# Kernel optimization log

Measured on AMD Instinct MI355X. Metric: run time of the kernel, lower is better.

## Reference

```python
import jax, jax.numpy as jnp
import numpy as np

N_NODES = 100000
N_EDGES = 400000
N_GRAPHS = 4096
D = 300          # emb_dim
L = 5            # num_layers
NUM_ATOM, NUM_CHIR = 120, 3
NUM_BOND, NUM_DIR = 6, 3
SELF_LOOP_BOND = 4
TEMP = 0.04


def setup_inputs() -> dict:
    key = jax.random.key(0)
    ks = jax.random.split(key, 24)
    inp = {}
    # graph batch 0
    inp["x0"] = jax.random.randint(ks[0], (N_NODES, 2), 0, 3)
    inp["edge_index0"] = jax.random.randint(ks[1], (2, N_EDGES), 0, N_NODES)
    inp["edge_attr0"] = jax.random.randint(ks[2], (N_EDGES, 2), 0, 3)
    inp["batch_ids0"] = jnp.sort(jax.random.randint(ks[3], (N_NODES,), 0, N_GRAPHS))
    inp["dangling0"] = jax.random.randint(ks[4], (N_GRAPHS,), 0, N_NODES)
    # graph batch 1
    inp["x1"] = jax.random.randint(ks[5], (N_NODES, 2), 0, 3)
    inp["edge_index1"] = jax.random.randint(ks[6], (2, N_EDGES), 0, N_NODES)
    inp["edge_attr1"] = jax.random.randint(ks[7], (N_EDGES, 2), 0, 3)
    inp["batch_ids1"] = jnp.sort(jax.random.randint(ks[8], (N_NODES,), 0, N_GRAPHS))
    inp["dangling1"] = jax.random.randint(ks[9], (N_GRAPHS,), 0, N_NODES)
    # shared encoder parameters
    g = lambda i, shp, s=0.1: (jax.random.normal(ks[i], shp, jnp.float32) * s)
    inp["atom_emb1"] = g(10, (NUM_ATOM, D))
    inp["atom_emb2"] = g(11, (NUM_CHIR, D))
    inp["eemb1"] = g(12, (L, NUM_BOND, D))
    inp["eemb2"] = g(13, (L, NUM_DIR, D))
    inp["W1"] = g(14, (L, D, 2 * D))
    inp["b1"] = jnp.zeros((L, 2 * D), jnp.float32)
    inp["W2"] = g(15, (L, 2 * D, D))
    inp["b2"] = jnp.zeros((L, D), jnp.float32)
    inp["bn_g"] = jnp.ones((L, D), jnp.float32)
    inp["bn_b"] = jnp.zeros((L, D), jnp.float32)
    # projectors stacked: 0=projector0, 1=projector1, 2=dangling_proj0, 3=dangling_proj1
    inp["pW1"] = g(16, (4, D, D))
    inp["pb1"] = jnp.zeros((4, D), jnp.float32)
    inp["pW2"] = g(17, (4, D, D))
    inp["pb2"] = jnp.zeros((4, D), jnp.float32)
    return inp


def _encode(x, edge_index, edge_attr, atom_emb1, atom_emb2,
            eemb1, eemb2, W1, b1, W2, b2, bn_g, bn_b):
    # initial node embedding: sum of atom-type and chirality embeddings
    h = atom_emb1[x[:, 0]] + atom_emb2[x[:, 1]]          # [N, D]
    src, dst = edge_index[0], edge_index[1]
    for l in range(L):
        e = eemb1[l][edge_attr[:, 0]] + eemb2[l][edge_attr[:, 1]]  # [E, D]
        msg = h[src] + e                                           # [E, D]
        agg = jax.ops.segment_sum(msg, dst, num_segments=h.shape[0])
        # self-loop with bond type 4, direction 0 (pretrain-gnns GINConv)
        agg = agg + h + eemb1[l][SELF_LOOP_BOND] + eemb2[l][0]
        z = jax.nn.relu(agg @ W1[l] + b1[l]) @ W2[l] + b2[l]       # GIN MLP
        mu = jnp.mean(z, axis=0)
        var = jnp.var(z, axis=0)
        z = (z - mu) * jax.lax.rsqrt(var + 1e-5) * bn_g[l] + bn_b[l]
        h = z if l == L - 1 else jax.nn.relu(z)                    # no ReLU on last layer
    return h


def _mlp(x, w1, bb1, w2, bb2):
    return jax.nn.relu(x @ w1 + bb1) @ w2 + bb2


def _branch(h, batch_ids, dangling, proj_i, dproj_i, pW1, pb1, pW2, pb2):
    pooled = jax.ops.segment_sum(h, batch_ids, num_segments=N_GRAPHS)
    counts = jax.ops.segment_sum(jnp.ones((h.shape[0],), h.dtype), batch_ids,
                                 num_segments=N_GRAPHS)
    pooled = pooled / jnp.maximum(counts, 1.0)[:, None]            # global_mean_pool
    out = _mlp(pooled, pW1[proj_i], pb1[proj_i], pW2[proj_i], pb2[proj_i])
    out = out + _mlp(h[dangling], pW1[dproj_i], pb1[dproj_i], pW2[dproj_i], pb2[dproj_i])
    return out / jnp.linalg.norm(out, axis=1, keepdims=True)       # L2 normalize


def reference(x0, edge_index0, edge_attr0, batch_ids0, dangling0,
              x1, edge_index1, edge_attr1, batch_ids1, dangling1,
              atom_emb1, atom_emb2, eemb1, eemb2, W1, b1, W2, b2, bn_g, bn_b,
              pW1, pb1, pW2, pb2):
    h0 = _encode(x0, edge_index0, edge_attr0, atom_emb1, atom_emb2,
                 eemb1, eemb2, W1, b1, W2, b2, bn_g, bn_b)
    f0 = _branch(h0, batch_ids0, dangling0, 0, 2, pW1, pb1, pW2, pb2)
    h1 = _encode(x1, edge_index1, edge_attr1, atom_emb1, atom_emb2,
                 eemb1, eemb2, W1, b1, W2, b2, bn_g, bn_b)
    f1 = _branch(h1, batch_ids1, dangling1, 1, 3, pW1, pb1, pW2, pb2)
    logits = (f0 @ f1.T) / TEMP                                    # [G, G]
    return logits
```

## Files before the change

### kernel.cpp

```cpp
#include <hip/hip_runtime.h>

#define NN    100000
#define NE    400000
#define NG    4096
#define LL    5
#define MPAD  100096
#define NCHUNK 98

typedef unsigned short u16;
typedef __attribute__((ext_vector_type(8))) _Float16 half8;
typedef __attribute__((ext_vector_type(4))) _Float16 hv4;
typedef __attribute__((ext_vector_type(4))) float float4v;
typedef __attribute__((ext_vector_type(16))) float float16v;
typedef __attribute__((ext_vector_type(8))) short short8v;

__device__ __forceinline__ float b2f(u16 u){
  union { float f; unsigned u; } c; c.u = ((unsigned)u)<<16; return c.f;
}
__device__ __forceinline__ u16 f2b(float f){
  union { float f; unsigned u; } c; c.f = f;
  unsigned x = c.u;
  return (u16)((x + 0x7fffu + ((x>>16)&1u)) >> 16);
}
__device__ __forceinline__ float h2f(u16 u){
  union { u16 s; _Float16 h; } c; c.s = u; return (float)c.h;
}
__device__ __forceinline__ u16 f2h(float f){
  union { u16 s; _Float16 h; } c; c.h = (_Float16)f; return c.s;
}
__device__ __forceinline__ void g2l16(const u16* g, u16* l){
  __builtin_amdgcn_global_load_lds((const __attribute__((address_space(1))) void*)g,
                                   (__attribute__((address_space(3))) void*)l, 16, 0, 0);
}

__global__ __launch_bounds__(256) void detect_dtype(const u16* __restrict__ p, int* __restrict__ flag){
  int i = blockIdx.x*256 + threadIdx.x;
  float v = b2f(p[i]);
  if (!(fabsf(v) <= 1e4f)) atomicOr(flag, 1);
}
__global__ __launch_bounds__(256) void cvt_param(const void* __restrict__ src, u16* __restrict__ dst,
                                                 int n, const int* __restrict__ flag){
  int i = blockIdx.x*256 + threadIdx.x;
  if (i >= n) return;
  float v = (*flag) ? ((const float*)src)[i] : b2f(((const u16*)src)[i]);
  dst[i] = f2h(v);
}

__global__ __launch_bounds__(256) void zero32(unsigned* __restrict__ p, int n){
  int i = blockIdx.x*256 + threadIdx.x;
  if (i < n) p[i] = 0u;
}

__global__ __launch_bounds__(256) void tpad(const u16* __restrict__ src, u16* __restrict__ dst,
                                            int L, int K, int N, int Kp, int Np){
  int idx = blockIdx.x*256 + threadIdx.x;
  if (idx >= L*Np*Kp) return;
  int l = idx/(Np*Kp); int r = idx - l*Np*Kp; int n = r/Kp; int k = r - n*Kp;
  dst[idx] = (n<N && k<K) ? src[(l*K + k)*N + n] : (u16)0;
}

__global__ __launch_bounds__(256) void ecomb_build(const u16* __restrict__ ee1, const u16* __restrict__ ee2,
                                                   u16* __restrict__ ec){
  int idx = blockIdx.x*256 + threadIdx.x;
  if (idx >= LL*18*160) return;
  int l = idx/(18*160); int r = idx - l*18*160; int c = r/160; int p = r - c*160;
  int a0 = c/3, a1 = c - a0*3;
  u16 o0=0,o1=0;
  if (p < 150){
    int d = 2*p;
    o0 = f2h(h2f(ee1[(l*6+a0)*300+d  ]) + h2f(ee2[(l*3+a1)*300+d  ]));
    o1 = f2h(h2f(ee1[(l*6+a0)*300+d+1]) + h2f(ee2[(l*3+a1)*300+d+1]));
  }
  ((ushort2*)ec)[idx] = make_ushort2(o0,o1);
}

__global__ __launch_bounds__(256) void node_init(const int* __restrict__ x, const u16* __restrict__ ae1,
                                                 const u16* __restrict__ ae2, u16* __restrict__ h){
  int idx = blockIdx.x*256 + threadIdx.x;
  if (idx >= MPAD*160) return;
  int n = idx/160, p = idx - n*160;
  u16 o0=0,o1=0;
  if (n < NN && p < 150){
    int a = x[2*n], ch = x[2*n+1];
    int d = 2*p;
    o0 = f2h(h2f(ae1[a*300+d  ]) + h2f(ae2[ch*300+d  ]));
    o1 = f2h(h2f(ae1[a*300+d+1]) + h2f(ae2[ch*300+d+1]));
  }
  ((ushort2*)h)[idx] = make_ushort2(o0,o1);
}

__global__ __launch_bounds__(256) void hist(const int* __restrict__ ei, int* __restrict__ counts){
  int e = blockIdx.x*256 + threadIdx.x;
  if (e >= NE) return;
  atomicAdd(&counts[ei[NE + e]], 1);
}
__global__ __launch_bounds__(256) void scan_chunks(const int* __restrict__ counts, int* __restrict__ csums){
  __shared__ int sd[256];
  int base = blockIdx.x*1024;
  int s = 0;
  for (int i = threadIdx.x; i < 1024; i += 256){ int g = base+i; if (g < NN) s += counts[g]; }
  sd[threadIdx.x] = s; __syncthreads();
  for (int off=128; off>0; off>>=1){ if (threadIdx.x < off) sd[threadIdx.x] += sd[threadIdx.x+off]; __syncthreads(); }
  if (threadIdx.x == 0) csums[blockIdx.x] = sd[0];
}
__global__ __launch_bounds__(128) void scan_base(const int* __restrict__ csums, int* __restrict__ cbase,
                                                 int* __restrict__ offsets){
  __shared__ int sd[128];
  int tid = threadIdx.x;
  int v = (tid < NCHUNK) ? csums[tid] : 0;
  sd[tid] = v; __syncthreads();
  for (int off=1; off<128; off<<=1){
    int t = (tid >= off) ? sd[tid-off] : 0; __syncthreads();
    sd[tid] += t; __syncthreads();
  }
  if (tid < NCHUNK) cbase[tid] = sd[tid] - v;
  if (tid == 0) offsets[NN] = sd[NCHUNK-1];
}
__global__ __launch_bounds__(256) void scan_final(const int* __restrict__ counts, const int* __restrict__ cbase,
                                                  int* __restrict__ offsets){
  __shared__ int sd[256];
  int tid = threadIdx.x;
  int base = blockIdx.x*1024 + tid*4;
  int v0 = (base   < NN) ? counts[base  ] : 0;
  int v1 = (base+1 < NN) ? counts[base+1] : 0;
  int v2 = (base+2 < NN) ? counts[base+2] : 0;
  int v3 = (base+3 < NN) ? counts[base+3] : 0;
  int s = v0+v1+v2+v3;
  sd[tid] = s; __syncthreads();
  for (int off=1; off<256; off<<=1){
    int t = (tid >= off) ? sd[tid-off] : 0; __syncthreads();
    sd[tid] += t; __syncthreads();
  }
  int run = cbase[blockIdx.x] + sd[tid] - s;
  if (base   < NN){ offsets[base  ] = run; } run += v0;
  if (base+1 < NN){ offsets[base+1] = run; } run += v1;
  if (base+2 < NN){ offsets[base+2] = run; } run += v2;
  if (base+3 < NN){ offsets[base+3] = run; }
}
__global__ __launch_bounds__(256) void fill_perm(const int* __restrict__ ei, const int* __restrict__ ea,
                                                 const int* __restrict__ offsets,
                                                 int* __restrict__ cursor, int* __restrict__ pk){
  int e = blockIdx.x*256 + threadIdx.x;
  if (e >= NE) return;
  int d = ei[NE + e];
  int src = ei[e];
  int c = ea[2*e]*3 + ea[2*e+1];
  int pos = offsets[d] + atomicAdd(&cursor[d], 1);
  pk[pos] = src*32 + c;
}

__global__ __launch_bounds__(256) void aggregate(
    const u16* __restrict__ h, const u16* __restrict__ ecL,
    const int* __restrict__ offsets, const int* __restrict__ pk,
    u16* __restrict__ agg)
{
  __shared__ u16 ecs[18*320];
  for (int i = threadIdx.x; i < 18*160; i += 256)
    ((ushort2*)ecs)[i] = ((const ushort2*)ecL)[i];
  __syncthreads();
  int node = blockIdx.x*4 + (threadIdx.x>>6);
  int lane = threadIdx.x & 63;
  bool tl = lane < 16;
  const hv4* h4 = (const hv4*)h;
  const hv4* e4 = (const hv4*)ecs;
  long base = (long)node*80;
  hv4 acc0, acc1 = (hv4)(_Float16)0;
  acc0 = h4[base + lane] + e4[12*80 + lane];
  if (tl) acc1 = h4[base + 64 + lane] + e4[12*80 + 64 + lane];
  if (node < NN){
    int s = offsets[node], en = offsets[node+1];
    int i = s;
    while (i + 3 < en){
      int p0 = pk[i], p1 = pk[i+1], p2 = pk[i+2], p3 = pk[i+3]; i += 4;
      long b0 = (long)(p0>>5)*80, b1 = (long)(p1>>5)*80;
      long b2 = (long)(p2>>5)*80, b3 = (long)(p3>>5)*80;
      int c0 = (p0&31)*80, c1 = (p1&31)*80, c2 = (p2&31)*80, c3 = (p3&31)*80;
      hv4 a0 = h4[b0+lane], a1 = h4[b1+lane], a2 = h4[b2+lane], a3 = h4[b3+lane];
      hv4 e0 = e4[c0+lane], e1 = e4[c1+lane], e2 = e4[c2+lane], e3 = e4[c3+lane];
      acc0 += (a0+e0); acc0 += (a1+e1); acc0 += (a2+e2); acc0 += (a3+e3);
      if (tl){
        hv4 x0 = h4[b0+64+lane], x1 = h4[b1+64+lane];
        hv4 x2 = h4[b2+64+lane], x3 = h4[b3+64+lane];
        hv4 y0 = e4[c0+64+lane], y1 = e4[c1+64+lane];
        hv4 y2 = e4[c2+64+lane], y3 = e4[c3+64+lane];
        acc1 += (x0+y0); acc1 += (x1+y1); acc1 += (x2+y2); acc1 += (x3+y3);
      }
    }
    while (i < en){
      int p0 = pk[i]; ++i;
      long b0 = (long)(p0>>5)*80; int c0 = (p0&31)*80;
      acc0 += (h4[b0+lane] + e4[c0+lane]);
      if (tl) acc1 += (h4[b0+64+lane] + e4[c0+64+lane]);
    }
  }
  hv4* a4 = (hv4*)agg;
  __builtin_nontemporal_store(acc0, &a4[base + lane]);
  if (tl) __builtin_nontemporal_store(acc1, &a4[base + 64 + lane]);
}

__global__ __launch_bounds__(512, 2) void gin_mlp(
    const u16* __restrict__ A,
    const u16* __restrict__ W1Tl,
    const u16* __restrict__ b1l,
    const u16* __restrict__ W2Tl,
    const u16* __restrict__ b2l,
    u16* __restrict__ Z,
    float* __restrict__ colsum, float* __restrict__ colsumsq)
{
  __shared__ __align__(16) u16 lds[32768];
  u16* uS = lds;
  u16* Ws = lds + 8192;
  int tid = threadIdx.x;
  int wave = tid>>6, lane = tid&63;
  int n5 = lane & 31, hi = lane >> 5;
  int q = lane>>4, r = lane&15;
  int rg = wave>>1, ch = wave&1;
  int wr = wave>>2, wc = wave&3;
  int m0 = blockIdx.x*128;

  half8 aReg[20];
  const u16* Arow = A + (long)(m0 + rg*32 + n5)*320 + hi*8;
  #pragma unroll
  for (int kc=0; kc<20; ++kc) aReg[kc] = *(const half8*)(Arow + kc*16);

  float4v zacc[4][6];
  #pragma unroll
  for (int i=0;i<4;i++)
    #pragma unroll
    for (int j=0;j<6;j++) zacc[i][j] = (float4v){0.f,0.f,0.f,0.f};

  for (int t1=0; t1<10; ++t1){
    int n1_0 = t1*64;
    __syncthreads();
    #pragma unroll
    for (int rnd=0; rnd<5; ++rnd){
      int ck = rnd*512 + tid;
      int n = ck/41, k8 = ck - n*41;
      const u16* src = (k8 < 40) ? (W1Tl + (long)(n1_0 + n)*320 + k8*8) : W1Tl;
      g2l16(src, Ws + ck*8);
    }
    if (tid < 64){
      int ck = 2560 + tid;
      int n = ck/41, k8 = ck - n*41;
      const u16* src = (k8 < 40) ? (W1Tl + (long)(n1_0 + n)*320 + k8*8) : W1Tl;
      g2l16(src, Ws + ck*8);
    }
    __syncthreads();
    float16v uacc = (float16v)(0.f);
    #pragma unroll
    for (int kc=0; kc<20; ++kc){
      half8 bw = *(const half8*)&Ws[(ch*32 + n5)*328 + kc*16 + hi*8];
      uacc = __builtin_amdgcn_mfma_f32_32x32x16_f16(aReg[kc], bw, uacc, 0,0,0);
    }
    {
      int n1g = n1_0 + ch*32 + n5;
      float bv = (n1g < 600) ? h2f(b1l[n1g]) : 0.f;
      u16* uw = uS + ch*4096 + n5;
      #pragma unroll
      for (int reg=0; reg<16; ++reg){
        int row = rg*32 + (reg&3) + 8*(reg>>2) + 4*hi;
        float v = fmaxf(uacc[reg] + bv, 0.f);
        uw[row*32] = f2h(v);
      }
    }
    __syncthreads();
    #pragma unroll
    for (int i=0;i<6;i++){
      int idx = tid*8 + i*4096;
      int kc2 = idx / 12288;
      int rem = idx - kc2*12288;
      int n2 = rem >> 5, k8 = rem & 31;
      g2l16(W2Tl + (long)n2*640 + n1_0 + kc2*32 + k8, Ws + idx);
    }
    __syncthreads();
    #pragma unroll
    for (int kc2=0; kc2<2; ++kc2){
      half8 af[4], bf[6];
      #pragma unroll
      for (int i=0;i<4;i++) af[i] = *(const half8*)&uS[kc2*4096 + (wr*64+i*16+r)*32 + q*8];
      #pragma unroll
      for (int j=0;j<6;j++) bf[j] = *(const half8*)&Ws[kc2*12288 + (wc*96+j*16+r)*32 + q*8];
      #pragma unroll
      for (int i=0;i<4;i++)
        #pragma unroll
        for (int j=0;j<6;j++)
          zacc[i][j] = __builtin_amdgcn_mfma_f32_16x16x32_f16(af[i], bf[j], zacc[i][j], 0,0,0);
    }
  }
  #pragma unroll
  for (int j=0;j<6;j++){
    int c = wc*96 + j*16 + r;
    float bv = (c < 300) ? h2f(b2l[c]) : 0.f;
    float s1 = 0.f, s2 = 0.f;
    #pragma unroll
    for (int i=0;i<4;i++){
      int rowb = m0 + wr*64 + i*16 + q*4;
      #pragma unroll
      for (int t=0;t<4;t++){
        float v = zacc[i][j][t] + bv;
        int gr = rowb + t;
        if (c < 320) __builtin_nontemporal_store(f2h(v), &Z[(long)gr*320 + c]);
        if (gr < NN){ s1 += v; s2 += v*v; }
      }
    }
    s1 += __shfl_xor(s1,16); s1 += __shfl_xor(s1,32);
    s2 += __shfl_xor(s2,16); s2 += __shfl_xor(s2,32);
    if (q == 0 && c < 384){ atomicAdd(&colsum[c], s1); atomicAdd(&colsumsq[c], s2); }
  }
}

__global__ __launch_bounds__(256) void gemm_nt(
    const u16* __restrict__ A, int lda,
    const u16* __restrict__ BT, int ldb,
    int Kp,
    const u16* __restrict__ bias, int Nreal,
    float scale, int dorelu, int omode, int Ncap,
    void* __restrict__ Cv, int ldc,
    const int* __restrict__ outmode)
{
  __shared__ __align__(16) u16 As[3][128*32];
  __shared__ __align__(16) u16 Bs[3][128*32];
  int tid = threadIdx.x;
  int wave = tid>>6, lane = tid&63;
  int wr = (wave>>1)&1, wc = wave&1;
  int nwg  = gridDim.x*gridDim.y;
  int flat = blockIdx.y*gridDim.x + blockIdx.x;
  int qd = nwg>>3, rm = nwg&7;
  int xcd = flat&7, sub = flat>>3;
  int wgid = (xcd<rm ? xcd*(qd+1) : rm*(qd+1)+(xcd-rm)*qd) + sub;
  int nt = wgid % gridDim.x, mt = wgid / gridDim.x;
  int m0 = mt*128, n0 = nt*128;
  int q = lane>>4, r = lane&15;
  int srow = tid>>2, scol = (tid&3)*8;
  const u16* Ag0 = A  + (long)(m0+srow)*lda + scol;
  const u16* Ag1 = A  + (long)(m0+64+srow)*lda + scol;
  const u16* Bg0 = BT + (long)(n0+srow)*ldb + scol;
  const u16* Bg1 = BT + (long)(n0+64+srow)*ldb + scol;
  float4v acc[4][4];
  #pragma unroll
  for (int i=0;i<4;i++)
    #pragma unroll
    for (int j=0;j<4;j++) acc[i][j] = (float4v){0.f,0.f,0.f,0.f};

  int nk = Kp >> 5;
  {
    g2l16(Ag0, &As[0][tid*8]);     g2l16(Ag1, &As[0][2048+tid*8]);
    g2l16(Bg0, &Bs[0][tid*8]);     g2l16(Bg1, &Bs[0][2048+tid*8]);
    if (nk > 1){
      g2l16(Ag0+32, &As[1][tid*8]);  g2l16(Ag1+32, &As[1][2048+tid*8]);
      g2l16(Bg0+32, &Bs[1][tid*8]);  g2l16(Bg1+32, &Bs[1][2048+tid*8]);
    }
  }
  for (int t=0; t<nk; ++t){
    int cur = t % 3;
    if (t+1 < nk) asm volatile("s_waitcnt vmcnt(4)" ::: "memory");
    else          asm volatile("s_waitcnt vmcnt(0)" ::: "memory");
    __builtin_amdgcn_s_barrier();
    if (t+2 < nk){
      int b = (t+2)%3, k0 = (t+2)*32;
      g2l16(Ag0+k0, &As[b][tid*8]);  g2l16(Ag1+k0, &As[b][2048+tid*8]);
      g2l16(Bg0+k0, &Bs[b][tid*8]);  g2l16(Bg1+k0, &Bs[b][2048+tid*8]);
    }
    half8 af[4], bf[4];
    #pragma unroll
    for (int i=0;i<4;i++) af[i] = *(const half8*)&As[cur][(wr*64+i*16+r)*32 + q*8];
    #pragma unroll
    for (int j=0;j<4;j++) bf[j] = *(const half8*)&Bs[cur][(wc*64+j*16+r)*32 + q*8];
    #pragma unroll
    for (int i=0;i<4;i++)
      #pragma unroll
      for (int j=0;j<4;j++)
        acc[i][j] = __builtin_amdgcn_mfma_f32_16x16x32_f16(af[i], bf[j], acc[i][j], 0,0,0);
  }

  int ob = omode;
  if (outmode) ob = (*outmode) ? 0 : 1;
  u16* Ch = (u16*)Cv; float* Cf = (float*)Cv;
  #pragma unroll
  for (int j=0;j<4;j++){
    int c = n0 + wc*64 + j*16 + r;
    float bv = (bias && c < Nreal) ? h2f(bias[c]) : 0.f;
    #pragma unroll
    for (int i=0;i<4;i++){
      int rowb = m0 + wr*64 + i*16 + q*4;
      #pragma unroll
      for (int tt=0; tt<4; ++tt){
        float v = acc[i][j][tt] + bv;
        if (dorelu) v = fmaxf(v, 0.f);
        v *= scale;
        int gr = rowb + tt;
        if (c < Ncap){
          long o = (long)gr*ldc + c;
          if (ob == 2)      Ch[o] = f2h(v);
          else if (ob == 1) Ch[o] = f2b(v);
          else              Cf[o] = v;
        }
      }
    }
  }
}

__global__ __launch_bounds__(320) void bn_finalize(const float* __restrict__ st, const u16* __restrict__ g,
                                                   const u16* __restrict__ b, float* __restrict__ sc,
                                                   float* __restrict__ sh){
  int c = threadIdx.x;
  if (c >= 300) return;
  float mu  = st[c] * (1.0f/NN);
  float var = st[384+c] * (1.0f/NN) - mu*mu;
  float inv = rsqrtf(var + 1e-5f);
  float gg = h2f(g[c]) * inv;
  sc[c] = gg; sh[c] = h2f(b[c]) - mu*gg;
}
__global__ __launch_bounds__(256) void bn_apply(const u16* __restrict__ z, const float* __restrict__ sc,
                                                const float* __restrict__ sh, u16* __restrict__ h, int dorelu){
  int idx = blockIdx.x*256 + threadIdx.x;
  if (idx >= NN*40) return;
  int n = idx/40, p = idx - n*40;
  short8v zz = ((const short8v*)z)[(long)n*40 + p];
  short8v out;
  #pragma unroll
  for (int e=0; e<8; ++e){
    int d = p*8 + e;
    float v = h2f((u16)zz[e])*sc[d] + sh[d];
    if (dorelu) v = fmaxf(v, 0.f);
    out[e] = (short)f2h(v);
    if (d >= 300) out[e] = 0;
  }
  ((short8v*)h)[(long)n*40 + p] = out;
}

__global__ __launch_bounds__(256) void graph_starts(const int* __restrict__ ids, int* __restrict__ starts){
  int i = blockIdx.x*256 + threadIdx.x;
  if (i >= NN) return;
  int b = ids[i];
  if (i == 0){ for (int g=0; g<=b; ++g) starts[g] = 0; }
  else { int p = ids[i-1]; for (int g=p+1; g<=b; ++g) starts[g] = i; }
  if (i == NN-1){ for (int g=b+1; g<=NG; ++g) starts[g] = NN; }
}
__global__ __launch_bounds__(256) void pool_kernel(const u16* __restrict__ h, const int* __restrict__ starts,
                                                   u16* __restrict__ pooled){
  int g = blockIdx.x*4 + (threadIdx.x>>6);
  int lane = threadIdx.x & 63;
  if (g >= NG) return;
  int s = starts[g], e = starts[g+1];
  int cnt = e - s; if (cnt < 1) cnt = 1;
  float inv = 1.0f/(float)cnt;
  float ax[3] = {0,0,0}, ay[3] = {0,0,0};
  const ushort2* h2 = (const ushort2*)h;
  for (int row=s; row<e; ++row){
    long base = (long)row*160;
    #pragma unroll
    for (int jp=0; jp<3; ++jp){
      int p = jp*64 + lane;
      if (p < 160){ ushort2 v = h2[base+p]; ax[jp] += h2f(v.x); ay[jp] += h2f(v.y); }
    }
  }
  ushort2* o2 = (ushort2*)pooled;
  #pragma unroll
  for (int jp=0; jp<3; ++jp){
    int p = jp*64 + lane;
    if (p < 160) o2[g*160+p] = make_ushort2(f2h(ax[jp]*inv), f2h(ay[jp]*inv));
  }
}
__global__ __launch_bounds__(256) void gather_rows(const u16* __restrict__ h, const int* __restrict__ idxs,
                                                   u16* __restrict__ out){
  int idx = blockIdx.x*256 + threadIdx.x;
  if (idx >= NG*160) return;
  int g = idx/160, p = idx - g*160;
  ((ushort2*)out)[idx] = ((const ushort2*)h)[(long)idxs[g]*160 + p];
}
__global__ __launch_bounds__(256) void add_norm(const float* __restrict__ vp, const float* __restrict__ vd,
                                                u16* __restrict__ f){
  int g = blockIdx.x*4 + (threadIdx.x>>6);
  int lane = threadIdx.x & 63;
  if (g >= NG) return;
  float vals[5]; float ss = 0.f;
  #pragma unroll
  for (int t=0; t<5; ++t){
    int d = lane + 64*t; float v = 0.f;
    if (d < 300) v = vp[g*320+d] + vd[g*320+d];
    vals[t] = v; ss += v*v;
  }
  #pragma unroll
  for (int off=32; off>0; off>>=1) ss += __shfl_xor(ss, off);
  float inv = rsqrtf(ss);
  #pragma unroll
  for (int t=0; t<5; ++t){
    int d = lane + 64*t;
    if (d < 320) f[g*320+d] = f2h(d < 300 ? vals[t]*inv : 0.f);
  }
}

extern "C" void kernel_launch(void* const* d_in, const int* in_sizes, int n_in,
                              void* d_out, int out_size, void* d_ws, size_t ws_size,
                              hipStream_t stream)
{
  const int* xin[2]  = {(const int*)d_in[0], (const int*)d_in[5]};
  const int* ei[2]   = {(const int*)d_in[1], (const int*)d_in[6]};
  const int* ea[2]   = {(const int*)d_in[2], (const int*)d_in[7]};
  const int* bid[2]  = {(const int*)d_in[3], (const int*)d_in[8]};
  const int* dang[2] = {(const int*)d_in[4], (const int*)d_in[9]};
  (void)in_sizes; (void)n_in; (void)out_size; (void)ws_size;

  char* w = (char*)d_ws;
  auto alloc = [&](size_t bytes)->char* {
    char* p = w; w += (bytes + 255) & ~(size_t)255; return p;
  };
  u16* hA   = (u16*)alloc((size_t)MPAD*320*2);
  u16* agg  = (u16*)alloc((size_t)MPAD*320*2);
  u16* z    = agg;
  u16*   pooled = (u16*)alloc((size_t)NG*320*2);
  u16*   hd     = (u16*)alloc((size_t)NG*320*2);
  u16*   ubuf   = (u16*)alloc((size_t)NG*384*2);
  float* vpb    = (float*)alloc((size_t)NG*320*4);
  float* vdb    = (float*)alloc((size_t)NG*320*4);
  u16* ec   = (u16*)alloc((size_t)LL*18*320*2);
  u16* W1T  = (u16*)alloc((size_t)LL*640*320*2);
  u16* W2T  = (u16*)alloc((size_t)LL*384*640*2);
  u16* pW1T = (u16*)alloc((size_t)4*384*320*2);
  u16* pW2T = (u16*)alloc((size_t)4*384*384*2);
  int* counts = (int*)alloc((size_t)NN*4);
  int* cursor = (int*)alloc((size_t)NN*4);
  int* offs   = (int*)alloc((size_t)(NN+1)*4);
  int* perm   = (int*)alloc((size_t)NE*4);
  int* csums  = (int*)alloc(512);
  int* cbase  = (int*)alloc(512);
  float* stats = (float*)alloc(768*4);
  float* bnsc  = (float*)alloc(384*4);
  float* bnsh  = (float*)alloc(384*4);
  int* starts  = (int*)alloc((size_t)(NG+1)*4);
  u16* f0b     = (u16*)alloc((size_t)NG*320*2);
  u16* f1b     = (u16*)alloc((size_t)NG*320*2);
  int* dflag   = (int*)alloc(256);
  const int pcnt[14] = {36000, 900, 9000, 4500, 900000, 3000, 900000, 1500,
                        1500, 1500, 360000, 1200, 360000, 1200};
  u16* parena = (u16*)alloc((size_t)2580300*2 + 14*256);
  u16* pp[14];
  { size_t off = 0;
    for (int i=0;i<14;i++){ pp[i] = parena + off; off += (size_t)((pcnt[i]+127)&~127); } }
  u16* ae1 = pp[0];  u16* ae2 = pp[1];  u16* ee1 = pp[2];  u16* ee2 = pp[3];
  u16* W1  = pp[4];  u16* b1  = pp[5];  u16* W2  = pp[6];  u16* b2  = pp[7];
  u16* bng = pp[8];  u16* bnb = pp[9];  u16* pW1 = pp[10]; u16* pb1 = pp[11];
  u16* pW2 = pp[12]; u16* pb2 = pp[13];

  auto cdiv = [](long a, long b){ return (int)((a + b - 1)/b); };
  auto gemm = [&](const u16* A, int lda, const u16* BT, int ldb, int Kp,
                  const u16* bias, int Nreal, float scale, int relu, int omode, int Ncap,
                  void* C, int ldc, int gx, int gy, const int* om){
    gemm_nt<<<dim3(gx,gy), 256, 0, stream>>>(A,lda,BT,ldb,Kp,bias,Nreal,scale,relu,omode,Ncap,
                                             C,ldc,om);
  };

  zero32<<<1,256,0,stream>>>((unsigned*)dflag, 1);
  detect_dtype<<<16,256,0,stream>>>((const u16*)d_in[14], dflag);
  for (int i=0;i<14;i++)
    cvt_param<<<cdiv(pcnt[i],256),256,0,stream>>>(d_in[10+i], pp[i], pcnt[i], dflag);

  tpad<<<cdiv((long)LL*640*320,256),256,0,stream>>>(W1,  W1T,  LL, 300, 600, 320, 640);
  tpad<<<cdiv((long)LL*384*640,256),256,0,stream>>>(W2,  W2T,  LL, 600, 300, 640, 384);
  tpad<<<cdiv((long)4*384*320,256),256,0,stream>>>(pW1, pW1T, 4,  300, 300, 320, 384);
  tpad<<<cdiv((long)4*384*384,256),256,0,stream>>>(pW2, pW2T, 4,  300, 300, 384, 384);
  ecomb_build<<<cdiv((long)LL*18*160,256),256,0,stream>>>(ee1, ee2, ec);

  for (int br=0; br<2; ++br){
    u16* fo = br ? f1b : f0b;
    node_init<<<cdiv((long)MPAD*160,256),256,0,stream>>>(xin[br], ae1, ae2, hA);
    zero32<<<cdiv(NN,256),256,0,stream>>>((unsigned*)counts, NN);
    hist<<<cdiv(NE,256),256,0,stream>>>(ei[br], counts);
    scan_chunks<<<NCHUNK,256,0,stream>>>(counts, csums);
    scan_base<<<1,128,0,stream>>>(csums, cbase, offs);
    scan_final<<<NCHUNK,256,0,stream>>>(counts, cbase, offs);
    zero32<<<cdiv(NN,256),256,0,stream>>>((unsigned*)cursor, NN);
    fill_perm<<<cdiv(NE,256),256,0,stream>>>(ei[br], ea[br], offs, cursor, perm);

    for (int l=0; l<LL; ++l){
      aggregate<<<MPAD/4,256,0,stream>>>(hA, ec + (size_t)l*18*320, offs, perm, agg);
      zero32<<<3,256,0,stream>>>((unsigned*)stats, 768);
      gin_mlp<<<MPAD/128, 512, 0, stream>>>(agg,
          W1T + (size_t)l*640*320, b1 + l*600,
          W2T + (size_t)l*384*640, b2 + l*300,
          z, stats, stats+384);
      bn_finalize<<<1,320,0,stream>>>(stats, bng + l*300, bnb + l*300, bnsc, bnsh);
      bn_apply<<<cdiv((long)NN*40,256),256,0,stream>>>(z, bnsc, bnsh, hA, (l < LL-1) ? 1 : 0);
    }

    graph_starts<<<cdiv(NN,256),256,0,stream>>>(bid[br], starts);
    pool_kernel<<<NG/4,256,0,stream>>>(hA, starts, pooled);
    gather_rows<<<cdiv((long)NG*160,256),256,0,stream>>>(hA, dang[br], hd);

    int pi = br, dpi = 2 + br;
    gemm(pooled, 320, pW1T + (size_t)pi*384*320, 320, 320,
         pb1 + pi*300, 300, 1.f, 1, 2, 384, ubuf, 384, 3, NG/128, nullptr);
    gemm(ubuf, 384, pW2T + (size_t)pi*384*384, 384, 384,
         pb2 + pi*300, 300, 1.f, 0, 0, 320, vpb, 320, 3, NG/128, nullptr);
    gemm(hd, 320, pW1T + (size_t)dpi*384*320, 320, 320,
         pb1 + dpi*300, 300, 1.f, 1, 2, 384, ubuf, 384, 3, NG/128, nullptr);
    gemm(ubuf, 384, pW2T + (size_t)dpi*384*384, 384, 384,
         pb2 + dpi*300, 300, 1.f, 0, 0, 320, vdb, 320, 3, NG/128, nullptr);
    add_norm<<<NG/4,256,0,stream>>>(vpb, vdb, fo);
  }

  gemm(f0b, 320, f1b, 320, 320, nullptr, 0, 25.0f, 0, 1, NG,
       d_out, NG, NG/128, NG/128, dflag);
}
```

Baseline: 3.547 ms.

## Double-buffer W1/W2 tiles in fused GIN MLP with async prefetch

```diff
diff --git a/kernel.cpp b/kernel.cpp
--- a/kernel.cpp
+++ b/kernel.cpp
@@ -11,7 +11,6 @@
 typedef __attribute__((ext_vector_type(8))) _Float16 half8;
 typedef __attribute__((ext_vector_type(4))) _Float16 hv4;
 typedef __attribute__((ext_vector_type(4))) float float4v;
-typedef __attribute__((ext_vector_type(16))) float float16v;
 typedef __attribute__((ext_vector_type(8))) short short8v;
 
 __device__ __forceinline__ float b2f(u16 u){
@@ -207,21 +206,27 @@
     u16* __restrict__ Z,
     float* __restrict__ colsum, float* __restrict__ colsumsq)
 {
-  __shared__ __align__(16) u16 lds[32768];
-  u16* uS = lds;
-  u16* Ws = lds + 8192;
+  extern __shared__ __align__(16) u16 lds[];
+  u16* uS     = lds;
+  u16* W1base = lds + 5120;
+  u16* W2base = lds + 5120 + 24576;
   int tid = threadIdx.x;
   int wave = tid>>6, lane = tid&63;
-  int n5 = lane & 31, hi = lane >> 5;
   int q = lane>>4, r = lane&15;
   int rg = wave>>1, ch = wave&1;
   int wr = wave>>2, wc = wave&3;
   int m0 = blockIdx.x*128;
 
-  half8 aReg[20];
-  const u16* Arow = A + (long)(m0 + rg*32 + n5)*320 + hi*8;
-  #pragma unroll
-  for (int kc=0; kc<20; ++kc) aReg[kc] = *(const half8*)(Arow + kc*16);
+  half8 aReg0[10], aReg1[10];
+  {
+    const u16* Arow0 = A + (long)(m0 + rg*32 + r)*320 + q*8;
+    const u16* Arow1 = A + (long)(m0 + rg*32 + 16 + r)*320 + q*8;
+    #pragma unroll
+    for (int kc=0; kc<10; ++kc){
+      aReg0[kc] = *(const half8*)(Arow0 + kc*32);
+      aReg1[kc] = *(const half8*)(Arow1 + kc*32);
+    }
+  }
 
   float4v zacc[4][6];
   #pragma unroll
@@ -229,64 +234,79 @@
     #pragma unroll
     for (int j=0;j<6;j++) zacc[i][j] = (float4v){0.f,0.f,0.f,0.f};
 
-  for (int t1=0; t1<10; ++t1){
-    int n1_0 = t1*64;
-    __syncthreads();
-    #pragma unroll
-    for (int rnd=0; rnd<5; ++rnd){
+  auto stageW1 = [&](int t, int buf){
+    int n1_0 = t*32;
+    u16* dst = W1base + buf*12288;
+    #pragma unroll
+    for (int rnd=0; rnd<3; ++rnd){
       int ck = rnd*512 + tid;
       int n = ck/41, k8 = ck - n*41;
-      const u16* src = (k8 < 40) ? (W1Tl + (long)(n1_0 + n)*320 + k8*8) : W1Tl;
-      g2l16(src, Ws + ck*8);
-    }
-    if (tid < 64){
-      int ck = 2560 + tid;
-      int n = ck/41, k8 = ck - n*41;
-      const u16* src = (k8 < 40) ? (W1Tl + (long)(n1_0 + n)*320 + k8*8) : W1Tl;
-      g2l16(src, Ws + ck*8);
-    }
-    __syncthreads();
-    float16v uacc = (float16v)(0.f);
-    #pragma unroll
-    for (int kc=0; kc<20; ++kc){
-      half8 bw = *(const half8*)&Ws[(ch*32 + n5)*328 + kc*16 + hi*8];
-      uacc = __builtin_amdgcn_mfma_f32_32x32x16_f16(aReg[kc], bw, uacc, 0,0,0);
-    }
+      bool real = (ck < 1312) && (k8 < 40);
+      const u16* src = real ? (W1Tl + (long)(n1_0 + n)*320 + k8*8) : W1Tl;
+      g2l16(src, dst + ck*8);
+    }
+  };
+  auto stageW2 = [&](int t, int buf){
+    int n1_0 = t*32;
+    u16* dst = W2base + buf*12288;
+    #pragma unroll
+    for (int rnd=0; rnd<3; ++rnd){
+      int i = rnd*512 + tid;
+      int n2 = i>>2, k8 = (i&3)*8;
+      g2l16(W2Tl + (long)n2*640 + n1_0 + k8, dst + i*8);
+    }
+  };
+
+  stageW1(0, 0);
+  stageW2(0, 0);
+  asm volatile("s_waitcnt vmcnt(0)" ::: "memory");
+  __builtin_amdgcn_s_barrier();
+
+  for (int t1=0; t1<20; ++t1){
+    int cb = t1 & 1, nb = cb ^ 1;
+    const u16* W1c = W1base + cb*12288;
+    const u16* W2c = W2base + cb*12288;
+    if (t1 < 19){ stageW1(t1+1, nb); stageW2(t1+1, nb); }
+
+    float4v ua0 = (float4v){0.f,0.f,0.f,0.f}, ua1 = (float4v){0.f,0.f,0.f,0.f};
+    __builtin_amdgcn_s_setprio(1);
+    #pragma unroll
+    for (int kc=0; kc<10; ++kc){
+      half8 bw = *(const half8*)&W1c[(ch*16 + r)*328 + kc*32 + q*8];
+      ua0 = __builtin_amdgcn_mfma_f32_16x16x32_f16(aReg0[kc], bw, ua0, 0,0,0);
+      ua1 = __builtin_amdgcn_mfma_f32_16x16x32_f16(aReg1[kc], bw, ua1, 0,0,0);
+    }
+    __builtin_amdgcn_s_setprio(0);
     {
-      int n1g = n1_0 + ch*32 + n5;
-      float bv = (n1g < 600) ? h2f(b1l[n1g]) : 0.f;
-      u16* uw = uS + ch*4096 + n5;
+      int n1c = t1*32 + ch*16 + r;
+      float bv = (n1c < 600) ? h2f(b1l[n1c]) : 0.f;
+      u16* uw = uS + (rg*32 + q*4)*40 + ch*16 + r;
       #pragma unroll
-      for (int reg=0; reg<16; ++reg){
-        int row = rg*32 + (reg&3) + 8*(reg>>2) + 4*hi;
-        float v = fmaxf(uacc[reg] + bv, 0.f);
-        uw[row*32] = f2h(v);
+      for (int reg=0; reg<4; ++reg){
+        uw[reg*40]       = f2h(fmaxf(ua0[reg] + bv, 0.f));
+        uw[640 + reg*40] = f2h(fmaxf(ua1[reg] + bv, 0.f));
       }
     }
-    __syncthreads();
-    #pragma unroll
-    for (int i=0;i<6;i++){
-      int idx = tid*8 + i*4096;
-      int kc2 = idx / 12288;
-      int rem = idx - kc2*12288;
-      int n2 = rem >> 5, k8 = rem & 31;
-      g2l16(W2Tl + (long)n2*640 + n1_0 + kc2*32 + k8, Ws + idx);
-    }
-    __syncthreads();
-    #pragma unroll
-    for (int kc2=0; kc2<2; ++kc2){
-      half8 af[4], bf[6];
+    asm volatile("s_waitcnt lgkmcnt(0)" ::: "memory");
+    __builtin_amdgcn_s_barrier();
+
+    half8 af[4], bf[6];
+    #pragma unroll
+    for (int i=0;i<4;i++) af[i] = *(const half8*)&uS[(wr*64 + i*16 + r)*40 + q*8];
+    #pragma unroll
+    for (int j=0;j<6;j++) bf[j] = *(const half8*)&W2c[(wc*96 + j*16 + r)*32 + q*8];
+    __builtin_amdgcn_s_setprio(1);
+    #pragma unroll
+    for (int i=0;i<4;i++)
       #pragma unroll
-      for (int i=0;i<4;i++) af[i] = *(const half8*)&uS[kc2*4096 + (wr*64+i*16+r)*32 + q*8];
-      #pragma unroll
-      for (int j=0;j<6;j++) bf[j] = *(const half8*)&Ws[kc2*12288 + (wc*96+j*16+r)*32 + q*8];
-      #pragma unroll
-      for (int i=0;i<4;i++)
-        #pragma unroll
-        for (int j=0;j<6;j++)
-          zacc[i][j] = __builtin_amdgcn_mfma_f32_16x16x32_f16(af[i], bf[j], zacc[i][j], 0,0,0);
-    }
-  }
+      for (int j=0;j<6;j++)
+        zacc[i][j] = __builtin_amdgcn_mfma_f32_16x16x32_f16(af[i], bf[j], zacc[i][j], 0,0,0);
+    __builtin_amdgcn_s_setprio(0);
+    asm volatile("s_waitcnt vmcnt(0)" ::: "memory");
+    asm volatile("s_waitcnt lgkmcnt(0)" ::: "memory");
+    __builtin_amdgcn_s_barrier();
+  }
+
   #pragma unroll
   for (int j=0;j<6;j++){
     int c = wc*96 + j*16 + r;
@@ -501,6 +521,13 @@
   const int* bid[2]  = {(const int*)d_in[3], (const int*)d_in[8]};
   const int* dang[2] = {(const int*)d_in[4], (const int*)d_in[9]};
   (void)in_sizes; (void)n_in; (void)out_size; (void)ws_size;
+
+  static bool ginAttrSet = false;
+  if (!ginAttrSet){
+    (void)hipFuncSetAttribute(reinterpret_cast<const void*>(gin_mlp),
+                              hipFuncAttributeMaxDynamicSharedMemorySize, 108544);
+    ginAttrSet = true;
+  }
 
   char* w = (char*)d_ws;
   auto alloc = [&](size_t bytes)->char* {
@@ -576,7 +603,7 @@
     for (int l=0; l<LL; ++l){
       aggregate<<<MPAD/4,256,0,stream>>>(hA, ec + (size_t)l*18*320, offs, perm, agg);
       zero32<<<3,256,0,stream>>>((unsigned*)stats, 768);
-      gin_mlp<<<MPAD/128, 512, 0, stream>>>(agg,
+      gin_mlp<<<MPAD/128, 512, 108544, stream>>>(agg,
           W1T + (size_t)l*640*320, b1 + l*600,
           W2T + (size_t)l*384*640, b2 + l*300,
           z, stats, stats+384);
```

Measured after the change: 3.673 ms. 1.04x slower.

## Fuse BatchNorm+ReLU of previous layer into aggregate gather

Applied to the files above, without the earlier changes.

```diff
diff --git a/kernel.cpp b/kernel.cpp
--- a/kernel.cpp
+++ b/kernel.cpp
@@ -152,7 +152,8 @@
 __global__ __launch_bounds__(256) void aggregate(
     const u16* __restrict__ h, const u16* __restrict__ ecL,
     const int* __restrict__ offsets, const int* __restrict__ pk,
-    u16* __restrict__ agg)
+    u16* __restrict__ agg,
+    const float* __restrict__ sc, const float* __restrict__ sh, int dobn)
 {
   __shared__ u16 ecs[18*320];
   for (int i = threadIdx.x; i < 18*160; i += 256)
@@ -161,12 +162,31 @@
   int node = blockIdx.x*4 + (threadIdx.x>>6);
   int lane = threadIdx.x & 63;
   bool tl = lane < 16;
+  hv4 s0 = (hv4)(_Float16)1, t0 = (hv4)(_Float16)0;
+  hv4 s1 = (hv4)(_Float16)1, t1 = (hv4)(_Float16)0;
+  if (dobn){
+    #pragma unroll
+    for (int j=0;j<4;++j){ s0[j] = (_Float16)sc[lane*4+j]; t0[j] = (_Float16)sh[lane*4+j]; }
+    if (tl){
+      #pragma unroll
+      for (int j=0;j<4;++j){ s1[j] = (_Float16)sc[256+lane*4+j]; t1[j] = (_Float16)sh[256+lane*4+j]; }
+    }
+  }
+  const hv4 hz = (hv4)(_Float16)0;
+  auto bn0 = [&](hv4 v)->hv4 {
+    if (!dobn) return v;
+    return __builtin_elementwise_max(v*s0 + t0, hz);
+  };
+  auto bn1 = [&](hv4 v)->hv4 {
+    if (!dobn) return v;
+    return __builtin_elementwise_max(v*s1 + t1, hz);
+  };
   const hv4* h4 = (const hv4*)h;
   const hv4* e4 = (const hv4*)ecs;
   long base = (long)node*80;
-  hv4 acc0, acc1 = (hv4)(_Float16)0;
-  acc0 = h4[base + lane] + e4[12*80 + lane];
-  if (tl) acc1 = h4[base + 64 + lane] + e4[12*80 + 64 + lane];
+  hv4 acc0, acc1 = hz;
+  acc0 = bn0(h4[base + lane]) + e4[12*80 + lane];
+  if (tl) acc1 = bn1(h4[base + 64 + lane]) + e4[12*80 + 64 + lane];
   if (node < NN){
     int s = offsets[node], en = offsets[node+1];
     int i = s;
@@ -175,12 +195,13 @@
       long b0 = (long)(p0>>5)*80, b1 = (long)(p1>>5)*80;
       long b2 = (long)(p2>>5)*80, b3 = (long)(p3>>5)*80;
       int c0 = (p0&31)*80, c1 = (p1&31)*80, c2 = (p2&31)*80, c3 = (p3&31)*80;
-      hv4 a0 = h4[b0+lane], a1 = h4[b1+lane], a2 = h4[b2+lane], a3 = h4[b3+lane];
+      hv4 a0 = bn0(h4[b0+lane]), a1 = bn0(h4[b1+lane]);
+      hv4 a2 = bn0(h4[b2+lane]), a3 = bn0(h4[b3+lane]);
       hv4 e0 = e4[c0+lane], e1 = e4[c1+lane], e2 = e4[c2+lane], e3 = e4[c3+lane];
       acc0 += (a0+e0); acc0 += (a1+e1); acc0 += (a2+e2); acc0 += (a3+e3);
       if (tl){
-        hv4 x0 = h4[b0+64+lane], x1 = h4[b1+64+lane];
-        hv4 x2 = h4[b2+64+lane], x3 = h4[b3+64+lane];
+        hv4 x0 = bn1(h4[b0+64+lane]), x1 = bn1(h4[b1+64+lane]);
+        hv4 x2 = bn1(h4[b2+64+lane]), x3 = bn1(h4[b3+64+lane]);
         hv4 y0 = e4[c0+64+lane], y1 = e4[c1+64+lane];
         hv4 y2 = e4[c2+64+lane], y3 = e4[c3+64+lane];
         acc1 += (x0+y0); acc1 += (x1+y1); acc1 += (x2+y2); acc1 += (x3+y3);
@@ -189,8 +210,8 @@
     while (i < en){
       int p0 = pk[i]; ++i;
       long b0 = (long)(p0>>5)*80; int c0 = (p0&31)*80;
-      acc0 += (h4[b0+lane] + e4[c0+lane]);
-      if (tl) acc1 += (h4[b0+64+lane] + e4[c0+64+lane]);
+      acc0 += (bn0(h4[b0+lane]) + e4[c0+lane]);
+      if (tl) acc1 += (bn1(h4[b0+64+lane]) + e4[c0+64+lane]);
     }
   }
   hv4* a4 = (hv4*)agg;
@@ -299,7 +320,7 @@
       for (int t=0;t<4;t++){
         float v = zacc[i][j][t] + bv;
         int gr = rowb + t;
-        if (c < 320) __builtin_nontemporal_store(f2h(v), &Z[(long)gr*320 + c]);
+        if (c < 320) Z[(long)gr*320 + c] = f2h(v);
         if (gr < NN){ s1 += v; s2 += v*v; }
       }
     }
@@ -404,7 +425,7 @@
                                                    const u16* __restrict__ b, float* __restrict__ sc,
                                                    float* __restrict__ sh){
   int c = threadIdx.x;
-  if (c >= 300) return;
+  if (c >= 300){ sc[c] = 0.f; sh[c] = 0.f; return; }
   float mu  = st[c] * (1.0f/NN);
   float var = st[384+c] * (1.0f/NN) - mu*mu;
   float inv = rsqrtf(var + 1e-5f);
@@ -506,9 +527,8 @@
   auto alloc = [&](size_t bytes)->char* {
     char* p = w; w += (bytes + 255) & ~(size_t)255; return p;
   };
-  u16* hA   = (u16*)alloc((size_t)MPAD*320*2);
-  u16* agg  = (u16*)alloc((size_t)MPAD*320*2);
-  u16* z    = agg;
+  u16* Zb   = (u16*)alloc((size_t)MPAD*320*2);
+  u16* Gb   = (u16*)alloc((size_t)MPAD*320*2);
   u16*   pooled = (u16*)alloc((size_t)NG*320*2);
   u16*   hd     = (u16*)alloc((size_t)NG*320*2);
   u16*   ubuf   = (u16*)alloc((size_t)NG*384*2);
@@ -564,7 +584,7 @@
 
   for (int br=0; br<2; ++br){
     u16* fo = br ? f1b : f0b;
-    node_init<<<cdiv((long)MPAD*160,256),256,0,stream>>>(xin[br], ae1, ae2, hA);
+    node_init<<<cdiv((long)MPAD*160,256),256,0,stream>>>(xin[br], ae1, ae2, Zb);
     zero32<<<cdiv(NN,256),256,0,stream>>>((unsigned*)counts, NN);
     hist<<<cdiv(NE,256),256,0,stream>>>(ei[br], counts);
     scan_chunks<<<NCHUNK,256,0,stream>>>(counts, csums);
@@ -574,19 +594,20 @@
     fill_perm<<<cdiv(NE,256),256,0,stream>>>(ei[br], ea[br], offs, cursor, perm);
 
     for (int l=0; l<LL; ++l){
-      aggregate<<<MPAD/4,256,0,stream>>>(hA, ec + (size_t)l*18*320, offs, perm, agg);
+      aggregate<<<MPAD/4,256,0,stream>>>(Zb, ec + (size_t)l*18*320, offs, perm, Gb,
+                                         bnsc, bnsh, (l > 0) ? 1 : 0);
       zero32<<<3,256,0,stream>>>((unsigned*)stats, 768);
-      gin_mlp<<<MPAD/128, 512, 0, stream>>>(agg,
+      gin_mlp<<<MPAD/128, 512, 0, stream>>>(Gb,
           W1T + (size_t)l*640*320, b1 + l*600,
           W2T + (size_t)l*384*640, b2 + l*300,
-          z, stats, stats+384);
+          Zb, stats, stats+384);
       bn_finalize<<<1,320,0,stream>>>(stats, bng + l*300, bnb + l*300, bnsc, bnsh);
-      bn_apply<<<cdiv((long)NN*40,256),256,0,stream>>>(z, bnsc, bnsh, hA, (l < LL-1) ? 1 : 0);
-    }
+    }
+    bn_apply<<<cdiv((long)NN*40,256),256,0,stream>>>(Zb, bnsc, bnsh, Gb, 0);
 
     graph_starts<<<cdiv(NN,256),256,0,stream>>>(bid[br], starts);
-    pool_kernel<<<NG/4,256,0,stream>>>(hA, starts, pooled);
-    gather_rows<<<cdiv((long)NG*160,256),256,0,stream>>>(hA, dang[br], hd);
+    pool_kernel<<<NG/4,256,0,stream>>>(Gb, starts, pooled);
+    gather_rows<<<cdiv((long)NG*160,256),256,0,stream>>>(Gb, dang[br], hd);
 
     int pi = br, dpi = 2 + br;
     gemm(pooled, 320, pW1T + (size_t)pi*384*320, 320, 320,
```

Result: no change. 3.559 ms (+0.3%).
